# Kernel tuning notes

Measured on AMD Instinct MI355X. Metric: run time of the kernel, lower is better.

The kernel has to match this reference:

```python
import jax, jax.numpy as jnp
import numpy as np

D_MODEL = 1024
NUM_HEADS = 16
D_K = D_MODEL // NUM_HEADS
BATCH = 4
SEQ = 2048


def setup_inputs() -> dict:
    key = jax.random.key(0)
    ks = jax.random.split(key, 12)
    s = 0.02
    inp = {
        "Q": jax.random.normal(ks[0], (BATCH, SEQ, D_MODEL), jnp.float32),
        "K": jax.random.normal(ks[1], (BATCH, SEQ, D_MODEL), jnp.float32),
        "V": jax.random.normal(ks[2], (BATCH, SEQ, D_MODEL), jnp.float32),
        "mask": jnp.tril(jnp.ones((SEQ, SEQ), jnp.int32)),  # causal: 0 = masked
        "Wq": jax.random.normal(ks[3], (D_MODEL, D_MODEL), jnp.float32) * s,
        "bq": jax.random.normal(ks[4], (D_MODEL,), jnp.float32) * s,
        "Wk": jax.random.normal(ks[5], (D_MODEL, D_MODEL), jnp.float32) * s,
        "bk": jax.random.normal(ks[6], (D_MODEL,), jnp.float32) * s,
        "Wv": jax.random.normal(ks[7], (D_MODEL, D_MODEL), jnp.float32) * s,
        "bv": jax.random.normal(ks[8], (D_MODEL,), jnp.float32) * s,
        "Wo": jax.random.normal(ks[9], (D_MODEL, D_MODEL), jnp.float32) * s,
        "bo": jax.random.normal(ks[10], (D_MODEL,), jnp.float32) * s,
    }
    return inp


def _split_heads(x):
    # (b, s, d_model) -> (b, h, s, d_k)
    b, s, _ = x.shape
    return x.reshape(b, s, NUM_HEADS, D_K).transpose(0, 2, 1, 3)


def reference(Q, K, V, mask, Wq, bq, Wk, bk, Wv, bv, Wo, bo):
    # Linear projections (torch Linear: x @ W^T + b)
    q = _split_heads(Q @ Wq.T + bq)  # (b, h, s, dk)
    k = _split_heads(K @ Wk.T + bk)
    v = _split_heads(V @ Wv.T + bv)
    scale = 1.0 / jnp.sqrt(jnp.asarray(D_K, q.dtype))
    scores = jnp.einsum("bhqd,bhkd->bhqk", q, k) * scale  # (b, h, s, s)
    scores = jnp.where(mask == 0, jnp.asarray(-jnp.inf, scores.dtype), scores)
    attn = jax.nn.softmax(scores, axis=-1)
    out = jnp.einsum("bhqk,bhkd->bhqd", attn, v)  # (b, h, s, dk)
    b, h, s, dk = out.shape
    out = out.transpose(0, 2, 1, 3).reshape(b, s, h * dk)  # combine heads
    return out @ Wo.T + bo
```

## Files before the change

### kernel.cpp

```cpp
#include <hip/hip_runtime.h>


typedef _Float16 f16;
typedef _Float16 f16x8 __attribute__((ext_vector_type(8)));
typedef _Float16 f16x4 __attribute__((ext_vector_type(4)));
typedef float floatx4 __attribute__((ext_vector_type(4)));
typedef float f32x16 __attribute__((ext_vector_type(16)));
typedef unsigned int uint4v __attribute__((ext_vector_type(4)));

#define SEQ 2048
#define DM 1024
#define NH 16
#define DK 64
#define MR 8192

#define QSCALE 0.18033688011112042f

#if __has_builtin(__builtin_amdgcn_exp2f)
#define EXP2(x) __builtin_amdgcn_exp2f(x)
#else
#define EXP2(x) __expf(0.6931471805599453f * (x))
#endif

__device__ __forceinline__ void gl_lds16(const void* g, void* lds) {
    __builtin_amdgcn_global_load_lds(
        (const __attribute__((address_space(1))) unsigned int*)g,
        (__attribute__((address_space(3))) unsigned int*)lds,
        16, 0, 0);
}

struct ConvArgs {
    const float* s[7];
    f16* d[7];
};

#define CONV_VBLOCKS (3 * 8192 + 4 * 1024)

__global__ __launch_bounds__(256) void convk(ConvArgs a) {
    for (int bx = blockIdx.x; bx < CONV_VBLOCKS; bx += (int)gridDim.x) {
        int t, base;
        if (bx < 3 * 8192) { t = bx / 8192; base = bx - t * 8192; }
        else { int r = bx - 3 * 8192; t = 3 + (r >> 10); base = r & 1023; }
        int i = base * 256 + threadIdx.x;
        float4 v = ((const float4*)a.s[t])[i];
        f16x4 o;
        o.x = (f16)v.x; o.y = (f16)v.y; o.z = (f16)v.z; o.w = (f16)v.w;
        ((f16x4*)a.d[t])[i] = o;
    }
}

template <int MODE>
__device__ __forceinline__ void gemm_body(
    const f16* __restrict__ A, const f16* __restrict__ W,
    const float* __restrict__ bias, void* __restrict__ outp,
    int m0, int n0, float oscale, f16* As, f16* Bs)
{
    const int tid = threadIdx.x;
    const int wave = tid >> 6, lane = tid & 63;
    const int quad = lane >> 4, ln = lane & 15;
    const int wr = wave >> 1, wc = wave & 1;

    floatx4 acc[4][4] = {};

    for (int kt = 0; kt < 16; ++kt) {
        const int k0 = kt * 64;
#pragma unroll
        for (int s = 0; s < 4; ++s) {
            int c = s * 256 + tid;
            int row = c >> 3, lc = (c & 7) ^ (row & 7);
            gl_lds16(A + (size_t)(m0 + row) * 1024 + k0 + lc * 8,
                     (char*)As + (s * 256 + wave * 64) * 16);
        }
#pragma unroll
        for (int s = 0; s < 4; ++s) {
            int c = s * 256 + tid;
            int row = c >> 3, lc = (c & 7) ^ (row & 7);
            gl_lds16(W + (size_t)(n0 + row) * 1024 + k0 + lc * 8,
                     (char*)Bs + (s * 256 + wave * 64) * 16);
        }
        __syncthreads();
#pragma unroll
        for (int kk = 0; kk < 64; kk += 32) {
            const int cb = kk >> 3;
            f16x8 af[4], bf[4];
#pragma unroll
            for (int i = 0; i < 4; ++i) {
                int row = wr * 64 + i * 16 + ln;
                af[i] = *(const f16x8*)&As[row * 64 + (((cb + quad) ^ (ln & 7)) << 3)];
            }
#pragma unroll
            for (int j = 0; j < 4; ++j) {
                int row = wc * 64 + j * 16 + ln;
                bf[j] = *(const f16x8*)&Bs[row * 64 + (((cb + quad) ^ (ln & 7)) << 3)];
            }
#pragma unroll
            for (int i = 0; i < 4; ++i)
#pragma unroll
                for (int j = 0; j < 4; ++j)
                    acc[i][j] = __builtin_amdgcn_mfma_f32_16x16x32_f16(
                        af[i], bf[j], acc[i][j], 0, 0, 0);
        }
        __syncthreads();
    }

#pragma unroll
    for (int i = 0; i < 4; ++i) {
#pragma unroll
        for (int j = 0; j < 4; ++j) {
            int col = n0 + wc * 64 + j * 16 + ln;
            float bc = bias[col];
            int rowb = m0 + wr * 64 + i * 16 + quad * 4;
            if (MODE == 1) {
                int bb = rowb >> 11, ss = rowb & 2047;
                int hh = col >> 6, dd = col & 63;
                f16x4 o4;
#pragma unroll
                for (int r = 0; r < 4; ++r)
                    o4[r] = (f16)((acc[i][j][r] + bc) * oscale);
                *(f16x4*)&((f16*)outp)[(((size_t)(bb * 16 + hh)) * 64 + dd) * 2048 + ss] = o4;
            } else {
#pragma unroll
                for (int r = 0; r < 4; ++r) {
                    float v = (acc[i][j][r] + bc) * oscale;
                    int rm = rowb + r;
                    if (MODE == 2) {
                        ((float*)outp)[(size_t)rm * 1024 + col] = v;
                    } else {
                        int bb = rm >> 11, ss = rm & 2047;
                        int hh = col >> 6, dd = col & 63;
                        ((f16*)outp)[(((size_t)(bb * 16 + hh)) * 2048 + ss) * 64 + dd] = (f16)v;
                    }
                }
            }
        }
    }
}

struct G3Args {
    const f16* A[3]; const f16* W[3]; const float* b[3]; f16* o[3];
};

__global__ __launch_bounds__(256, 2) void gemm_qkv(G3Args g) {
    __shared__ alignas(16) f16 As[128 * 64];
    __shared__ alignas(16) f16 Bs[128 * 64];
    const int z = blockIdx.z;
    const int m0 = blockIdx.x * 128, n0 = blockIdx.y * 128;
    if (z < 2)
        gemm_body<0>(g.A[z], g.W[z], g.b[z], g.o[z], m0, n0,
                     z == 0 ? QSCALE : 1.0f, As, Bs);
    else
        gemm_body<1>(g.A[2], g.W[2], g.b[2], g.o[2], m0, n0, 1.0f, As, Bs);
}

__global__ __launch_bounds__(256, 2) void gemm_out(
    const f16* __restrict__ A, const f16* __restrict__ W,
    const float* __restrict__ bias, float* __restrict__ outp)
{
    __shared__ alignas(16) f16 As[128 * 64];
    __shared__ alignas(16) f16 Bs[128 * 64];
    gemm_body<2>(A, W, bias, outp, blockIdx.x * 128, blockIdx.y * 128, 1.0f, As, Bs);
}

__global__ __launch_bounds__(256, 3) void attn_kernel(
    const f16* __restrict__ Qp, const f16* __restrict__ Kp,
    const f16* __restrict__ Vt, f16* __restrict__ Op)
{
    __shared__ alignas(16) f16 ks[128 * 64];
    __shared__ alignas(16) f16 vs[64 * 128];

    const int tid = threadIdx.x;
    const int wave = tid >> 6, lane = tid & 63;
    const int h = lane >> 5, c31 = lane & 31;
    const int bh = blockIdx.x;
    const f16* qb = Qp + (size_t)bh * SEQ * DK;
    const f16* kbp = Kp + (size_t)bh * SEQ * DK;
    const f16* vb = Vt + (size_t)bh * DK * SEQ;
    const int b = bh >> 4, hd = bh & 15;

    f16x8 ones;
#pragma unroll
    for (int e = 0; e < 8; ++e) ones[e] = (f16)1.0f;

    for (int half = 0; half < 2; ++half) {
        const int jt = half ? (15 - blockIdx.y) : blockIdx.y;
        const int q0 = jt * 128;

#pragma unroll
        for (int s = 0; s < 4; ++s) {
            int c = s * 256 + tid;
            int row = c >> 3, lc = (c & 7) ^ (row & 7);
            gl_lds16(qb + (size_t)(q0 + row) * 64 + lc * 8,
                     (char*)ks + (s * 256 + wave * 64) * 16);
        }
        __syncthreads();
        f16x8 bq[4];
#pragma unroll
        for (int t = 0; t < 4; ++t) {
            int row = wave * 32 + c31;
            bq[t] = *(const f16x8*)&ks[row * 64 + (((2 * t + h) ^ (row & 7)) << 3)];
        }
        __syncthreads();

        f32x16 oacc0 = {}, oacc1 = {}, lacc = {};

        const int nk = jt + 1;
        for (int kt = 0; kt < nk; ++kt) {
            const int k0 = kt * 128;
#pragma unroll
            for (int s = 0; s < 4; ++s) {
                int c = s * 256 + tid;
                int row = c >> 3, lc = (c & 7) ^ (row & 7);
                gl_lds16(kbp + (size_t)(k0 + row) * 64 + lc * 8,
                         (char*)ks + (s * 256 + wave * 64) * 16);
            }
#pragma unroll
            for (int s = 0; s < 4; ++s) {
                int c = s * 256 + tid;
                int row = c >> 4, lc = (c & 15) ^ (row & 15);
                gl_lds16(vb + (size_t)row * SEQ + k0 + lc * 8,
                         (char*)vs + (s * 256 + wave * 64) * 16);
            }
            __syncthreads();

            const bool diag = (kt == jt);
            const int qloc = wave * 32 + c31;

#pragma unroll
            for (int kb = 0; kb < 4; ++kb) {
                f32x16 sacc = {};
#pragma unroll
                for (int t = 0; t < 4; ++t) {
                    int row = kb * 32 + c31;
                    f16x8 ak = *(const f16x8*)&ks[row * 64 + (((2 * t + h) ^ (row & 7)) << 3)];
                    sacc = __builtin_amdgcn_mfma_f32_32x32x16_f16(
                        ak, bq[t], sacc, 0, 0, 0);
                }

                unsigned pg[4][2];
#pragma unroll
                for (int g = 0; g < 4; ++g) {
#pragma unroll
                    for (int j = 0; j < 2; ++j) {
                        const int r = 4 * g + 2 * j;
                        const int kg = kb * 32 + 8 * g + 4 * h + 2 * j;
                        float s0 = sacc[r], s1 = sacc[r + 1];
                        float p0 = (diag && kg > qloc) ? 0.0f : EXP2(s0);
                        float p1 = (diag && kg + 1 > qloc) ? 0.0f : EXP2(s1);
                        auto pp = __builtin_amdgcn_cvt_pkrtz(p0, p1);
                        pg[g][j] = __builtin_bit_cast(unsigned, pp);
                    }
                }

#pragma unroll
                for (int sub = 0; sub < 2; ++sub) {
                    const int s = 2 * kb + sub;
                    unsigned a0 = pg[2 * sub][0], a1 = pg[2 * sub][1];
                    unsigned b0 = pg[2 * sub + 1][0], b1 = pg[2 * sub + 1][1];
                    asm("v_permlane32_swap_b32 %0, %1" : "+v"(a0), "+v"(b0));
                    asm("v_permlane32_swap_b32 %0, %1" : "+v"(a1), "+v"(b1));
                    uint4v fw;
                    fw.x = a0; fw.y = a1; fw.z = b0; fw.w = b1;
                    f16x8 F = __builtin_bit_cast(f16x8, fw);

                    lacc = __builtin_amdgcn_mfma_f32_32x32x16_f16(
                        F, ones, lacc, 0, 0, 0);
                    {
                        int row = c31;
                        f16x8 bv = *(const f16x8*)&vs[row * 128 + (((2 * s + h) ^ (row & 15)) << 3)];
                        oacc0 = __builtin_amdgcn_mfma_f32_32x32x16_f16(
                            F, bv, oacc0, 0, 0, 0);
                    }
                    {
                        int row = 32 + c31;
                        f16x8 bv = *(const f16x8*)&vs[row * 128 + (((2 * s + h) ^ (row & 15)) << 3)];
                        oacc1 = __builtin_amdgcn_mfma_f32_32x32x16_f16(
                            F, bv, oacc1, 0, 0, 0);
                    }
                }
            }
            __syncthreads();
        }

#pragma unroll
        for (int r = 0; r < 16; ++r) {
            const int qr = (r & 3) + 8 * (r >> 2) + 4 * h;
            const int rowg = q0 + wave * 32 + qr;
            float inv = 1.0f / lacc[r];
            {
                int col = hd * 64 + c31;
                Op[((size_t)b * SEQ + rowg) * DM + col] = (f16)(oacc0[r] * inv);
            }
            {
                int col = hd * 64 + 32 + c31;
                Op[((size_t)b * SEQ + rowg) * DM + col] = (f16)(oacc1[r] * inv);
            }
        }
    }
}

extern "C" void kernel_launch(void* const* d_in, const int* in_sizes, int n_in,
                              void* d_out, int out_size, void* d_ws, size_t ws_size,
                              hipStream_t stream) {
    const float* Q  = (const float*)d_in[0];
    const float* K  = (const float*)d_in[1];
    const float* V  = (const float*)d_in[2];
    const float* Wq = (const float*)d_in[4];
    const float* bq = (const float*)d_in[5];
    const float* Wk = (const float*)d_in[6];
    const float* bk = (const float*)d_in[7];
    const float* Wv = (const float*)d_in[8];
    const float* bv = (const float*)d_in[9];
    const float* Wo = (const float*)d_in[10];
    const float* bo = (const float*)d_in[11];

    char* ws = (char*)d_ws;
    f16* Xq  = (f16*)(ws);
    f16* Xk  = Xq + (size_t)MR * DM;
    f16* Xv  = Xk + (size_t)MR * DM;
    f16* Wqb = Xv + (size_t)MR * DM;
    f16* Wkb = Wqb + (size_t)DM * DM;
    f16* Wvb = Wkb + (size_t)DM * DM;
    f16* Wob = Wvb + (size_t)DM * DM;
    f16* qp  = Wob + (size_t)DM * DM;
    f16* kp  = qp + (size_t)MR * DM;
    f16* vtp = kp + (size_t)MR * DM;

    ConvArgs ca;
    ca.s[0] = Q;  ca.d[0] = Xq;
    ca.s[1] = K;  ca.d[1] = Xk;
    ca.s[2] = V;  ca.d[2] = Xv;
    ca.s[3] = Wq; ca.d[3] = Wqb;
    ca.s[4] = Wk; ca.d[4] = Wkb;
    ca.s[5] = Wv; ca.d[5] = Wvb;
    ca.s[6] = Wo; ca.d[6] = Wob;
    convk<<<2048, 256, 0, stream>>>(ca);

    G3Args g;
    g.A[0] = Xq; g.W[0] = Wqb; g.b[0] = bq; g.o[0] = qp;
    g.A[1] = Xk; g.W[1] = Wkb; g.b[1] = bk; g.o[1] = kp;
    g.A[2] = Xv; g.W[2] = Wvb; g.b[2] = bv; g.o[2] = vtp;
    gemm_qkv<<<dim3(64, 8, 3), 256, 0, stream>>>(g);

    attn_kernel<<<dim3(64, 8), 256, 0, stream>>>(qp, kp, vtp, Xq);

    gemm_out<<<dim3(64, 8), 256, 0, stream>>>(Xq, Wob, bo, (float*)d_out);
}
```

Before: 307.8 us.

## Fuse fp32-to-fp16 activation conversion into QKV GEMM tile loads

The QKV projection GEMM now loads fp32 activation tiles directly into LDS and converts them to fp16 when building the MFMA fragments. The separate conversion pass over the Q, K and V activations is dropped, leaving only the weight conversion kernel. This removes a full read and write of three large activation tensors, but doubles LDS use for the A tile, which may lower occupancy. It also reloads fp32 data from global memory for every N-tile block and adds conversion instructions inside the inner loop.

```diff
diff --git a/kernel.cpp b/kernel.cpp
--- a/kernel.cpp
+++ b/kernel.cpp
@@ -7,6 +7,7 @@
 typedef float floatx4 __attribute__((ext_vector_type(4)));
 typedef float f32x16 __attribute__((ext_vector_type(16)));
 typedef unsigned int uint4v __attribute__((ext_vector_type(4)));
+typedef unsigned short u16x8 __attribute__((ext_vector_type(8)));
 
 #define SEQ 2048
 #define DM 1024
@@ -29,31 +30,32 @@
         16, 0, 0);
 }
 
+__device__ __forceinline__ unsigned short cvt_rne_u16(float x) {
+    unsigned int r;
+    asm("v_cvt_f16_f32 %0, %1" : "=v"(r) : "v"(x));
+    return (unsigned short)r;
+}
+
 struct ConvArgs {
-    const float* s[7];
-    f16* d[7];
+    const float* s[4];
+    f16* d[4];
 };
 
-#define CONV_VBLOCKS (3 * 8192 + 4 * 1024)
-
 __global__ __launch_bounds__(256) void convk(ConvArgs a) {
-    for (int bx = blockIdx.x; bx < CONV_VBLOCKS; bx += (int)gridDim.x) {
-        int t, base;
-        if (bx < 3 * 8192) { t = bx / 8192; base = bx - t * 8192; }
-        else { int r = bx - 3 * 8192; t = 3 + (r >> 10); base = r & 1023; }
-        int i = base * 256 + threadIdx.x;
-        float4 v = ((const float4*)a.s[t])[i];
-        f16x4 o;
-        o.x = (f16)v.x; o.y = (f16)v.y; o.z = (f16)v.z; o.w = (f16)v.w;
-        ((f16x4*)a.d[t])[i] = o;
-    }
-}
-
-template <int MODE>
+    int bx = blockIdx.x;
+    int t = bx >> 10, base = bx & 1023;
+    int i = base * 256 + threadIdx.x;
+    float4 v = ((const float4*)a.s[t])[i];
+    f16x4 o;
+    o.x = (f16)v.x; o.y = (f16)v.y; o.z = (f16)v.z; o.w = (f16)v.w;
+    ((f16x4*)a.d[t])[i] = o;
+}
+
+template <int MODE, bool AF32>
 __device__ __forceinline__ void gemm_body(
-    const f16* __restrict__ A, const f16* __restrict__ W,
+    const void* __restrict__ Ap, const f16* __restrict__ W,
     const float* __restrict__ bias, void* __restrict__ outp,
-    int m0, int n0, float oscale, f16* As, f16* Bs)
+    int m0, int n0, float oscale, void* As_raw, f16* Bs)
 {
     const int tid = threadIdx.x;
     const int wave = tid >> 6, lane = tid & 63;
@@ -64,12 +66,24 @@
 
     for (int kt = 0; kt < 16; ++kt) {
         const int k0 = kt * 64;
-#pragma unroll
-        for (int s = 0; s < 4; ++s) {
-            int c = s * 256 + tid;
-            int row = c >> 3, lc = (c & 7) ^ (row & 7);
-            gl_lds16(A + (size_t)(m0 + row) * 1024 + k0 + lc * 8,
-                     (char*)As + (s * 256 + wave * 64) * 16);
+        if constexpr (AF32) {
+            const float* Af = (const float*)Ap;
+#pragma unroll
+            for (int s = 0; s < 8; ++s) {
+                int c = s * 256 + tid;
+                int row = c >> 4, lc = (c & 15) ^ (row & 15);
+                gl_lds16(Af + (size_t)(m0 + row) * 1024 + k0 + lc * 4,
+                         (char*)As_raw + (s * 256 + wave * 64) * 16);
+            }
+        } else {
+            const f16* Ah = (const f16*)Ap;
+#pragma unroll
+            for (int s = 0; s < 4; ++s) {
+                int c = s * 256 + tid;
+                int row = c >> 3, lc = (c & 7) ^ (row & 7);
+                gl_lds16(Ah + (size_t)(m0 + row) * 1024 + k0 + lc * 8,
+                         (char*)As_raw + (s * 256 + wave * 64) * 16);
+            }
         }
 #pragma unroll
         for (int s = 0; s < 4; ++s) {
@@ -86,7 +100,23 @@
 #pragma unroll
             for (int i = 0; i < 4; ++i) {
                 int row = wr * 64 + i * 16 + ln;
-                af[i] = *(const f16x8*)&As[row * 64 + (((cb + quad) ^ (ln & 7)) << 3)];
+                if constexpr (AF32) {
+                    const float* Asf = (const float*)As_raw;
+                    const int j = cb + quad;
+                    const int p0 = (2 * j) ^ ln;
+                    const int p1 = (2 * j + 1) ^ ln;
+                    floatx4 lo = *(const floatx4*)&Asf[row * 64 + p0 * 4];
+                    floatx4 hi = *(const floatx4*)&Asf[row * 64 + p1 * 4];
+                    u16x8 u;
+                    u[0] = cvt_rne_u16(lo[0]); u[1] = cvt_rne_u16(lo[1]);
+                    u[2] = cvt_rne_u16(lo[2]); u[3] = cvt_rne_u16(lo[3]);
+                    u[4] = cvt_rne_u16(hi[0]); u[5] = cvt_rne_u16(hi[1]);
+                    u[6] = cvt_rne_u16(hi[2]); u[7] = cvt_rne_u16(hi[3]);
+                    af[i] = __builtin_bit_cast(f16x8, u);
+                } else {
+                    const f16* Ash = (const f16*)As_raw;
+                    af[i] = *(const f16x8*)&Ash[row * 64 + (((cb + quad) ^ (ln & 7)) << 3)];
+                }
             }
 #pragma unroll
             for (int j = 0; j < 4; ++j) {
@@ -137,19 +167,19 @@
 }
 
 struct G3Args {
-    const f16* A[3]; const f16* W[3]; const float* b[3]; f16* o[3];
+    const float* A[3]; const f16* W[3]; const float* b[3]; f16* o[3];
 };
 
 __global__ __launch_bounds__(256, 2) void gemm_qkv(G3Args g) {
-    __shared__ alignas(16) f16 As[128 * 64];
+    __shared__ alignas(16) float Asf[128 * 64];
     __shared__ alignas(16) f16 Bs[128 * 64];
     const int z = blockIdx.z;
     const int m0 = blockIdx.x * 128, n0 = blockIdx.y * 128;
     if (z < 2)
-        gemm_body<0>(g.A[z], g.W[z], g.b[z], g.o[z], m0, n0,
-                     z == 0 ? QSCALE : 1.0f, As, Bs);
+        gemm_body<0, true>(g.A[z], g.W[z], g.b[z], g.o[z], m0, n0,
+                           z == 0 ? QSCALE : 1.0f, Asf, Bs);
     else
-        gemm_body<1>(g.A[2], g.W[2], g.b[2], g.o[2], m0, n0, 1.0f, As, Bs);
+        gemm_body<1, true>(g.A[2], g.W[2], g.b[2], g.o[2], m0, n0, 1.0f, Asf, Bs);
 }
 
 __global__ __launch_bounds__(256, 2) void gemm_out(
@@ -158,7 +188,8 @@
 {
     __shared__ alignas(16) f16 As[128 * 64];
     __shared__ alignas(16) f16 Bs[128 * 64];
-    gemm_body<2>(A, W, bias, outp, blockIdx.x * 128, blockIdx.y * 128, 1.0f, As, Bs);
+    gemm_body<2, false>(A, W, bias, outp, blockIdx.x * 128, blockIdx.y * 128,
+                        1.0f, As, Bs);
 }
 
 __global__ __launch_bounds__(256, 3) void attn_kernel(
@@ -314,34 +345,29 @@
     const float* bo = (const float*)d_in[11];
 
     char* ws = (char*)d_ws;
-    f16* Xq  = (f16*)(ws);
-    f16* Xk  = Xq + (size_t)MR * DM;
-    f16* Xv  = Xk + (size_t)MR * DM;
-    f16* Wqb = Xv + (size_t)MR * DM;
+    f16* Wqb = (f16*)ws;
     f16* Wkb = Wqb + (size_t)DM * DM;
     f16* Wvb = Wkb + (size_t)DM * DM;
     f16* Wob = Wvb + (size_t)DM * DM;
     f16* qp  = Wob + (size_t)DM * DM;
     f16* kp  = qp + (size_t)MR * DM;
     f16* vtp = kp + (size_t)MR * DM;
+    f16* Ao  = vtp + (size_t)MR * DM;
 
     ConvArgs ca;
-    ca.s[0] = Q;  ca.d[0] = Xq;
-    ca.s[1] = K;  ca.d[1] = Xk;
-    ca.s[2] = V;  ca.d[2] = Xv;
-    ca.s[3] = Wq; ca.d[3] = Wqb;
-    ca.s[4] = Wk; ca.d[4] = Wkb;
-    ca.s[5] = Wv; ca.d[5] = Wvb;
-    ca.s[6] = Wo; ca.d[6] = Wob;
-    convk<<<2048, 256, 0, stream>>>(ca);
+    ca.s[0] = Wq; ca.d[0] = Wqb;
+    ca.s[1] = Wk; ca.d[1] = Wkb;
+    ca.s[2] = Wv; ca.d[2] = Wvb;
+    ca.s[3] = Wo; ca.d[3] = Wob;
+    convk<<<4 * 1024, 256, 0, stream>>>(ca);
 
     G3Args g;
-    g.A[0] = Xq; g.W[0] = Wqb; g.b[0] = bq; g.o[0] = qp;
-    g.A[1] = Xk; g.W[1] = Wkb; g.b[1] = bk; g.o[1] = kp;
-    g.A[2] = Xv; g.W[2] = Wvb; g.b[2] = bv; g.o[2] = vtp;
+    g.A[0] = Q; g.W[0] = Wqb; g.b[0] = bq; g.o[0] = qp;
+    g.A[1] = K; g.W[1] = Wkb; g.b[1] = bk; g.o[1] = kp;
+    g.A[2] = V; g.W[2] = Wvb; g.b[2] = bv; g.o[2] = vtp;
     gemm_qkv<<<dim3(64, 8, 3), 256, 0, stream>>>(g);
 
-    attn_kernel<<<dim3(64, 8), 256, 0, stream>>>(qp, kp, vtp, Xq);
-
-    gemm_out<<<dim3(64, 8), 256, 0, stream>>>(Xq, Wob, bo, (float*)d_out);
-}
+    attn_kernel<<<dim3(64, 8), 256, 0, stream>>>(qp, kp, vtp, Ao);
+
+    gemm_out<<<dim3(64, 8), 256, 0, stream>>>(Ao, Wob, bo, (float*)d_out);
+}
```

New measurement: 304.8 us. About the same (-1.0%).
